# Kernel optimization log

Measured on AMD Instinct MI355X. Metric: run time of the kernel, lower is better.

The kernel has to match this reference:

```python
import jax, jax.numpy as jnp
import numpy as np

D_MODEL = 1024
NUM_HEADS = 16
HEAD_DIM = D_MODEL // NUM_HEADS
B, S = 2, 2048


def setup_inputs() -> dict:
    key = jax.random.key(0)
    ks = jax.random.split(key, 7)
    scale = 1.0 / np.sqrt(D_MODEL)
    return {
        "query": jax.random.normal(ks[0], (B, S, D_MODEL), jnp.float32),
        "key": jax.random.normal(ks[1], (B, S, D_MODEL), jnp.float32),
        "value": jax.random.normal(ks[2], (B, S, D_MODEL), jnp.float32),
        "Wq": jax.random.normal(ks[3], (D_MODEL, D_MODEL), jnp.float32) * scale,
        "Wk": jax.random.normal(ks[4], (D_MODEL, D_MODEL), jnp.float32) * scale,
        "Wv": jax.random.normal(ks[5], (D_MODEL, D_MODEL), jnp.float32) * scale,
        "Wo": jax.random.normal(ks[6], (D_MODEL, D_MODEL), jnp.float32) * scale,
    }


def reference(query, key, value, Wq, Wk, Wv, Wo):
    b, tl, _ = query.shape
    sl = key.shape[1]
    # Linear (no bias): x @ W.T, then split heads -> (B, H, L, Dh)
    def split_heads(x, L):
        return x.reshape(b, L, NUM_HEADS, HEAD_DIM).transpose(0, 2, 1, 3)
    Q = split_heads(query @ Wq.T, tl)
    K = split_heads(key @ Wk.T, sl)
    V = split_heads(value @ Wv.T, sl)
    scores = jnp.einsum("bhqd,bhkd->bhqk", Q, K) / jnp.sqrt(jnp.float32(HEAD_DIM))
    attn_weights = jax.nn.softmax(scores, axis=-1)
    # dropout is identity in eval mode
    context = jnp.einsum("bhqk,bhkd->bhqd", attn_weights, V)
    context = context.transpose(0, 2, 1, 3).reshape(b, tl, D_MODEL)
    output = context @ Wo.T
    return (output, attn_weights)
```

## Files before the change

kernel.cpp:

```cpp
#include <hip/hip_runtime.h>
#include <stdint.h>
#include <stddef.h>

#define D_MODEL 1024
#define NHEADS  16
#define HDIM    64
#define BB      2
#define SSEQ    2048

using bf16x8 = __attribute__((ext_vector_type(8))) short;
using f32x4  = __attribute__((ext_vector_type(4))) float;
using s16x4  = __attribute__((ext_vector_type(4))) short;

static __device__ __forceinline__ float b2f(short s) {
  union { float f; unsigned u; } v;
  v.u = ((unsigned)(unsigned short)s) << 16;
  return v.f;
}
static __device__ __forceinline__ short f2b(float f) {
  union { float f; unsigned u; } v;
  v.f = f;
  unsigned r = v.u + 0x7fffu + ((v.u >> 16) & 1u);
  return (short)(r >> 16);
}

static __device__ __forceinline__ void gload16(const void* g, void* l) {
  __builtin_amdgcn_global_load_lds(
      (const __attribute__((address_space(1))) unsigned int*)g,
      (__attribute__((address_space(3))) unsigned int*)l, 16, 0, 0);
}

__global__ __launch_bounds__(256) void k_cvt(const float* __restrict__ src,
                                             short* __restrict__ dst, int n4) {
  int i = blockIdx.x * blockDim.x + threadIdx.x;
  const int stride = gridDim.x * blockDim.x;
  for (; i < n4; i += stride) {
    const float4 v = ((const float4*)src)[i];
    s16x4 o;
    o[0] = f2b(v.x); o[1] = f2b(v.y); o[2] = f2b(v.z); o[3] = f2b(v.w);
    ((s16x4*)dst)[i] = o;
  }
}

template <bool F32OUT>
static __device__ __forceinline__ void gemm_bt_dev(
    const short* __restrict__ A, const short* __restrict__ W, void* __restrict__ Cv,
    int N, int K) {
  __shared__ short sA[128 * 32];
  __shared__ short sB[128 * 32];

  const int t  = threadIdx.x;
  const int l  = t & 63;
  const int w  = t >> 6;
  const int wm = w >> 1, wn = w & 1;
  const int g  = l >> 4, lr = l & 15;
  const int m0 = blockIdx.y * 128;
  const int n0 = blockIdx.x * 128;

  f32x4 acc[4][4];
#pragma unroll
  for (int i = 0; i < 4; ++i)
#pragma unroll
    for (int j = 0; j < 4; ++j) {
      acc[i][j][0] = 0.f; acc[i][j][1] = 0.f;
      acc[i][j][2] = 0.f; acc[i][j][3] = 0.f;
    }

  const int r0 = t >> 2;
  const int c0 = (t & 3) * 8;
  const short* ga0 = A + (size_t)(m0 + r0) * K + c0;
  const short* ga1 = A + (size_t)(m0 + 64 + r0) * K + c0;
  const short* gb0 = W + (size_t)(n0 + r0) * K + c0;
  const short* gb1 = W + (size_t)(n0 + 64 + r0) * K + c0;
  short* la0 = &sA[(t & ~63) * 8];
  short* la1 = la0 + 256 * 8;
  short* lb0 = &sB[(t & ~63) * 8];
  short* lb1 = lb0 + 256 * 8;

  for (int k0 = 0; k0 < K; k0 += 32) {
    __syncthreads();
    gload16(ga0 + k0, la0);
    gload16(ga1 + k0, la1);
    gload16(gb0 + k0, lb0);
    gload16(gb1 + k0, lb1);
    __syncthreads();

    bf16x8 af[4], bfr[4];
#pragma unroll
    for (int i = 0; i < 4; ++i)
      af[i] = *(const bf16x8*)&sA[(wm * 64 + i * 16 + lr) * 32 + g * 8];
#pragma unroll
    for (int i = 0; i < 4; ++i)
      bfr[i] = *(const bf16x8*)&sB[(wn * 64 + i * 16 + lr) * 32 + g * 8];
#pragma unroll
    for (int i = 0; i < 4; ++i)
#pragma unroll
      for (int j = 0; j < 4; ++j)
        acc[i][j] = __builtin_amdgcn_mfma_f32_16x16x32_bf16(af[i], bfr[j],
                                                            acc[i][j], 0, 0, 0);
  }

#pragma unroll
  for (int i = 0; i < 4; ++i)
#pragma unroll
    for (int j = 0; j < 4; ++j)
#pragma unroll
      for (int rr = 0; rr < 4; ++rr) {
        const int row = m0 + wm * 64 + i * 16 + g * 4 + rr;
        const int col = n0 + wn * 64 + j * 16 + lr;
        if (F32OUT)
          ((float*)Cv)[(size_t)row * N + col] = acc[i][j][rr];
        else
          ((short*)Cv)[(size_t)row * N + col] = f2b(acc[i][j][rr]);
      }
}

__global__ __launch_bounds__(256) void k_gemm_f32out(
    const short* __restrict__ A, const short* __restrict__ W,
    float* __restrict__ C, int N, int K) {
  gemm_bt_dev<true>(A, W, C, N, K);
}

__global__ __launch_bounds__(256) void k_gemm_qkv(
    const short* __restrict__ q, const short* __restrict__ k,
    const short* __restrict__ v, const short* __restrict__ wq,
    const short* __restrict__ wk, const short* __restrict__ wv,
    short* __restrict__ Qb, short* __restrict__ Kb, short* __restrict__ Vb) {
  const short *A, *W;
  short* C;
  if (blockIdx.z == 0)      { A = q; W = wq; C = Qb; }
  else if (blockIdx.z == 1) { A = k; W = wk; C = Kb; }
  else                      { A = v; W = wv; C = Vb; }
  gemm_bt_dev<false>(A, W, C, D_MODEL, D_MODEL);
}

__global__ __launch_bounds__(256) void k_transpose_v(
    const short* __restrict__ Vb, short* __restrict__ Vt) {
  __shared__ short tile[64][66];
  const int bh = blockIdx.x;
  const int b = bh >> 4, h = bh & 15;
  const int s0 = blockIdx.y * 64;
  const int t = threadIdx.x;
#pragma unroll
  for (int i = 0; i < 16; ++i) {
    int e = t + i * 256;
    int si = e >> 6, dj = e & 63;
    tile[si][dj] = Vb[((size_t)b * SSEQ + s0 + si) * D_MODEL + h * HDIM + dj];
  }
  __syncthreads();
#pragma unroll
  for (int i = 0; i < 16; ++i) {
    int e = t + i * 256;
    int dj = e >> 6, si = e & 63;
    Vt[((size_t)bh * HDIM + dj) * SSEQ + s0 + si] = tile[si][dj];
  }
}

__global__ __launch_bounds__(512) void k_attn(
    const short* __restrict__ Qb, const short* __restrict__ Kb,
    const short* __restrict__ Vt, float* __restrict__ attnO,
    short* __restrict__ ctx) {
  __shared__ short S[16 * SSEQ];
  __shared__ f32x4 red[4 * 64];
  const int t = threadIdx.x;
  const int l = t & 63, w = t >> 6;
  const int g = l >> 4, lr = l & 15;
  const int bh = blockIdx.y;
  const int b = bh >> 4, h = bh & 15;
  const int q0 = blockIdx.x * 16;

  const size_t qoff = ((size_t)b * SSEQ + q0 + lr) * D_MODEL + h * HDIM;
  const bf16x8 aq0 = *(const bf16x8*)&Qb[qoff + g * 8];
  const bf16x8 aq1 = *(const bf16x8*)&Qb[qoff + 32 + g * 8];

  const short* Kh = Kb + (size_t)b * SSEQ * D_MODEL + h * HDIM;

  for (int nt = 0; nt < 16; ++nt) {
    const int n0 = (w * 16 + nt) * 16;
    const short* krow = Kh + (size_t)(n0 + lr) * D_MODEL;
    const bf16x8 bk0 = *(const bf16x8*)&krow[g * 8];
    const bf16x8 bk1 = *(const bf16x8*)&krow[32 + g * 8];
    f32x4 acc;
    acc[0] = 0.f; acc[1] = 0.f; acc[2] = 0.f; acc[3] = 0.f;
    acc = __builtin_amdgcn_mfma_f32_16x16x32_bf16(aq0, bk0, acc, 0, 0, 0);
    acc = __builtin_amdgcn_mfma_f32_16x16x32_bf16(aq1, bk1, acc, 0, 0, 0);
#pragma unroll
    for (int rr = 0; rr < 4; ++rr) {
      const int row = g * 4 + rr;
      const int col = n0 + lr;
      const int pc = (col >> 3) ^ (row & 7);
      S[row * SSEQ + pc * 8 + (col & 7)] = f2b(acc[rr] * 0.125f);
    }
  }
  __syncthreads();

  const int r = t >> 5, j = t & 31;
  float mx = -1e30f;
  for (int i = 0; i < 8; ++i) {
    const int c = j + (i << 5);
    const int pc = c ^ (r & 7);
    const bf16x8 v = *(const bf16x8*)&S[r * SSEQ + pc * 8];
#pragma unroll
    for (int e = 0; e < 8; ++e) mx = fmaxf(mx, b2f(v[e]));
  }
#pragma unroll
  for (int mask = 1; mask < 32; mask <<= 1)
    mx = fmaxf(mx, __shfl_xor(mx, mask, 64));

  float sum = 0.f;
  for (int i = 0; i < 8; ++i) {
    const int c = j + (i << 5);
    const int pc = c ^ (r & 7);
    const bf16x8 v = *(const bf16x8*)&S[r * SSEQ + pc * 8];
#pragma unroll
    for (int e = 0; e < 8; ++e) sum += __expf(b2f(v[e]) - mx);
  }
#pragma unroll
  for (int mask = 1; mask < 32; mask <<= 1) sum += __shfl_xor(sum, mask, 64);
  const float inv = 1.f / sum;

  float* arow = attnO + ((size_t)bh * SSEQ + q0 + r) * SSEQ;
  for (int i = 0; i < 8; ++i) {
    const int c = j + (i << 5);
    const int pc = c ^ (r & 7);
    const bf16x8 v = *(const bf16x8*)&S[r * SSEQ + pc * 8];
    bf16x8 p;
#pragma unroll
    for (int e = 0; e < 8; ++e) {
      const float pe = __expf(b2f(v[e]) - mx) * inv;
      p[e] = f2b(pe);
      arow[(size_t)c * 8 + e] = pe;
    }
    *(bf16x8*)&S[r * SSEQ + pc * 8] = p;
  }
  __syncthreads();

  const short* Vh = Vt + (size_t)bh * HDIM * SSEQ;
  const int d0 = (w & 3) * 16;
  const int kh = w >> 2;
  f32x4 acc;
  acc[0] = 0.f; acc[1] = 0.f; acc[2] = 0.f; acc[3] = 0.f;
  const int sbeg = kh * (SSEQ / 2);
  for (int s0 = sbeg; s0 < sbeg + SSEQ / 2; s0 += 32) {
    const int pc = ((s0 >> 3) + g) ^ (lr & 7);
    const bf16x8 ap = *(const bf16x8*)&S[lr * SSEQ + pc * 8];
    const bf16x8 bv =
        *(const bf16x8*)&Vh[(size_t)(d0 + lr) * SSEQ + s0 + g * 8];
    acc = __builtin_amdgcn_mfma_f32_16x16x32_bf16(ap, bv, acc, 0, 0, 0);
  }
  if (kh == 1) red[(w & 3) * 64 + l] = acc;
  __syncthreads();
  if (kh == 0) {
    const f32x4 o = red[(w & 3) * 64 + l];
    acc[0] += o[0]; acc[1] += o[1]; acc[2] += o[2]; acc[3] += o[3];
#pragma unroll
    for (int rr = 0; rr < 4; ++rr) {
      const int qr = q0 + g * 4 + rr;
      ctx[((size_t)b * SSEQ + qr) * D_MODEL + h * HDIM + d0 + lr] =
          f2b(acc[rr]);
    }
  }
}

extern "C" void kernel_launch(void* const* d_in, const int* in_sizes, int n_in,
                              void* d_out, int out_size, void* d_ws,
                              size_t ws_size, hipStream_t stream) {
  const float* qf  = (const float*)d_in[0];
  const float* kf  = (const float*)d_in[1];
  const float* vf  = (const float*)d_in[2];
  const float* wqf = (const float*)d_in[3];
  const float* wkf = (const float*)d_in[4];
  const float* wvf = (const float*)d_in[5];
  const float* wof = (const float*)d_in[6];

  float* out  = (float*)d_out;
  float* attn = out + (size_t)BB * SSEQ * D_MODEL;

  const size_t NTOK = (size_t)BB * SSEQ;
  const size_t XN = NTOK * D_MODEL;
  const size_t WN = (size_t)D_MODEL * D_MODEL;

  short* qb  = (short*)d_ws;
  short* kb  = qb + XN;
  short* vb  = kb + XN;
  short* wqb = vb + XN;
  short* wkb = wqb + WN;
  short* wvb = wkb + WN;
  short* wob = wvb + WN;
  short* Qb  = wob + WN;
  short* Kb  = Qb + XN;
  short* Vb  = Kb + XN;
  short* Vt  = Vb + XN;
  short* ctx = Vt + XN;

  k_cvt<<<512, 256, 0, stream>>>(qf, qb, (int)(XN / 4));
  k_cvt<<<512, 256, 0, stream>>>(kf, kb, (int)(XN / 4));
  k_cvt<<<512, 256, 0, stream>>>(vf, vb, (int)(XN / 4));
  k_cvt<<<256, 256, 0, stream>>>(wqf, wqb, (int)(WN / 4));
  k_cvt<<<256, 256, 0, stream>>>(wkf, wkb, (int)(WN / 4));
  k_cvt<<<256, 256, 0, stream>>>(wvf, wvb, (int)(WN / 4));
  k_cvt<<<256, 256, 0, stream>>>(wof, wob, (int)(WN / 4));

  k_gemm_qkv<<<dim3(D_MODEL / 128, NTOK / 128, 3), 256, 0, stream>>>(
      qb, kb, vb, wqb, wkb, wvb, Qb, Kb, Vb);
  k_transpose_v<<<dim3(BB * NHEADS, SSEQ / 64), 256, 0, stream>>>(Vb, Vt);
  k_attn<<<dim3(SSEQ / 16, BB * NHEADS), 512, 0, stream>>>(Qb, Kb, Vt, attn,
                                                           ctx);
  k_gemm_f32out<<<dim3(D_MODEL / 128, NTOK / 128), 256, 0, stream>>>(
      ctx, wob, out, D_MODEL, D_MODEL);
}
```

Measured before the change: 898.4 us.

## Remap attention blocks for XCD locality, fuse row max, vectorize stores, unroll PV

```diff
diff --git a/kernel.cpp b/kernel.cpp
--- a/kernel.cpp
+++ b/kernel.cpp
@@ -162,12 +162,15 @@
     short* __restrict__ ctx) {
   __shared__ short S[16 * SSEQ];
   __shared__ f32x4 red[4 * 64];
+  __shared__ float rowmax[16][8];
   const int t = threadIdx.x;
   const int l = t & 63, w = t >> 6;
   const int g = l >> 4, lr = l & 15;
-  const int bh = blockIdx.y;
+  const int orig = blockIdx.x;
+  const int id = (orig & 7) * 512 + (orig >> 3);
+  const int q0 = (id & 127) * 16;
+  const int bh = id >> 7;
   const int b = bh >> 4, h = bh & 15;
-  const int q0 = blockIdx.x * 16;
 
   const size_t qoff = ((size_t)b * SSEQ + q0 + lr) * D_MODEL + h * HDIM;
   const bf16x8 aq0 = *(const bf16x8*)&Qb[qoff + g * 8];
@@ -175,37 +178,49 @@
 
   const short* Kh = Kb + (size_t)b * SSEQ * D_MODEL + h * HDIM;
 
-  for (int nt = 0; nt < 16; ++nt) {
-    const int n0 = (w * 16 + nt) * 16;
-    const short* krow = Kh + (size_t)(n0 + lr) * D_MODEL;
-    const bf16x8 bk0 = *(const bf16x8*)&krow[g * 8];
-    const bf16x8 bk1 = *(const bf16x8*)&krow[32 + g * 8];
-    f32x4 acc;
-    acc[0] = 0.f; acc[1] = 0.f; acc[2] = 0.f; acc[3] = 0.f;
-    acc = __builtin_amdgcn_mfma_f32_16x16x32_bf16(aq0, bk0, acc, 0, 0, 0);
-    acc = __builtin_amdgcn_mfma_f32_16x16x32_bf16(aq1, bk1, acc, 0, 0, 0);
+  f32x4 pmax;
+  pmax[0] = -1e30f; pmax[1] = -1e30f; pmax[2] = -1e30f; pmax[3] = -1e30f;
+  for (int nt = 0; nt < 16; nt += 2) {
+    const int n0a = (w * 16 + nt) * 16;
+    const int n0b = n0a + 16;
+    const short* kra = Kh + (size_t)(n0a + lr) * D_MODEL;
+    const short* krb = Kh + (size_t)(n0b + lr) * D_MODEL;
+    const bf16x8 ka0 = *(const bf16x8*)&kra[g * 8];
+    const bf16x8 ka1 = *(const bf16x8*)&kra[32 + g * 8];
+    const bf16x8 kb0 = *(const bf16x8*)&krb[g * 8];
+    const bf16x8 kb1 = *(const bf16x8*)&krb[32 + g * 8];
+    f32x4 acca, accb;
+    acca[0] = 0.f; acca[1] = 0.f; acca[2] = 0.f; acca[3] = 0.f;
+    accb[0] = 0.f; accb[1] = 0.f; accb[2] = 0.f; accb[3] = 0.f;
+    acca = __builtin_amdgcn_mfma_f32_16x16x32_bf16(aq0, ka0, acca, 0, 0, 0);
+    acca = __builtin_amdgcn_mfma_f32_16x16x32_bf16(aq1, ka1, acca, 0, 0, 0);
+    accb = __builtin_amdgcn_mfma_f32_16x16x32_bf16(aq0, kb0, accb, 0, 0, 0);
+    accb = __builtin_amdgcn_mfma_f32_16x16x32_bf16(aq1, kb1, accb, 0, 0, 0);
 #pragma unroll
     for (int rr = 0; rr < 4; ++rr) {
       const int row = g * 4 + rr;
-      const int col = n0 + lr;
-      const int pc = (col >> 3) ^ (row & 7);
-      S[row * SSEQ + pc * 8 + (col & 7)] = f2b(acc[rr] * 0.125f);
-    }
-  }
+      const float sa = acca[rr] * 0.125f;
+      const float sb = accb[rr] * 0.125f;
+      pmax[rr] = fmaxf(pmax[rr], fmaxf(sa, sb));
+      const int ca = n0a + lr, cb = n0b + lr;
+      S[row * SSEQ + (((ca >> 3) ^ (row & 7)) << 3) + (ca & 7)] = f2b(sa);
+      S[row * SSEQ + (((cb >> 3) ^ (row & 7)) << 3) + (cb & 7)] = f2b(sb);
+    }
+  }
+#pragma unroll
+  for (int mask = 1; mask < 16; mask <<= 1)
+#pragma unroll
+    for (int rr = 0; rr < 4; ++rr)
+      pmax[rr] = fmaxf(pmax[rr], __shfl_xor(pmax[rr], mask, 64));
+  if (lr == 0)
+#pragma unroll
+    for (int rr = 0; rr < 4; ++rr) rowmax[g * 4 + rr][w] = pmax[rr];
   __syncthreads();
 
   const int r = t >> 5, j = t & 31;
-  float mx = -1e30f;
-  for (int i = 0; i < 8; ++i) {
-    const int c = j + (i << 5);
-    const int pc = c ^ (r & 7);
-    const bf16x8 v = *(const bf16x8*)&S[r * SSEQ + pc * 8];
-#pragma unroll
-    for (int e = 0; e < 8; ++e) mx = fmaxf(mx, b2f(v[e]));
-  }
-#pragma unroll
-  for (int mask = 1; mask < 32; mask <<= 1)
-    mx = fmaxf(mx, __shfl_xor(mx, mask, 64));
+  float mx = rowmax[r][0];
+#pragma unroll
+  for (int ww = 1; ww < 8; ++ww) mx = fmaxf(mx, rowmax[r][ww]);
 
   float sum = 0.f;
   for (int i = 0; i < 8; ++i) {
@@ -225,12 +240,23 @@
     const int pc = c ^ (r & 7);
     const bf16x8 v = *(const bf16x8*)&S[r * SSEQ + pc * 8];
     bf16x8 p;
-#pragma unroll
-    for (int e = 0; e < 8; ++e) {
-      const float pe = __expf(b2f(v[e]) - mx) * inv;
-      p[e] = f2b(pe);
-      arow[(size_t)c * 8 + e] = pe;
-    }
+    float4 w0, w1;
+    {
+      const float p0 = __expf(b2f(v[0]) - mx) * inv;
+      const float p1 = __expf(b2f(v[1]) - mx) * inv;
+      const float p2 = __expf(b2f(v[2]) - mx) * inv;
+      const float p3 = __expf(b2f(v[3]) - mx) * inv;
+      w0.x = p0; w0.y = p1; w0.z = p2; w0.w = p3;
+      p[0] = f2b(p0); p[1] = f2b(p1); p[2] = f2b(p2); p[3] = f2b(p3);
+      const float p4 = __expf(b2f(v[4]) - mx) * inv;
+      const float p5 = __expf(b2f(v[5]) - mx) * inv;
+      const float p6 = __expf(b2f(v[6]) - mx) * inv;
+      const float p7 = __expf(b2f(v[7]) - mx) * inv;
+      w1.x = p4; w1.y = p5; w1.z = p6; w1.w = p7;
+      p[4] = f2b(p4); p[5] = f2b(p5); p[6] = f2b(p6); p[7] = f2b(p7);
+    }
+    *(float4*)(arow + (size_t)c * 8) = w0;
+    *(float4*)(arow + (size_t)c * 8 + 4) = w1;
     *(bf16x8*)&S[r * SSEQ + pc * 8] = p;
   }
   __syncthreads();
@@ -241,12 +267,18 @@
   f32x4 acc;
   acc[0] = 0.f; acc[1] = 0.f; acc[2] = 0.f; acc[3] = 0.f;
   const int sbeg = kh * (SSEQ / 2);
-  for (int s0 = sbeg; s0 < sbeg + SSEQ / 2; s0 += 32) {
-    const int pc = ((s0 >> 3) + g) ^ (lr & 7);
-    const bf16x8 ap = *(const bf16x8*)&S[lr * SSEQ + pc * 8];
-    const bf16x8 bv =
-        *(const bf16x8*)&Vh[(size_t)(d0 + lr) * SSEQ + s0 + g * 8];
-    acc = __builtin_amdgcn_mfma_f32_16x16x32_bf16(ap, bv, acc, 0, 0, 0);
+  for (int s0 = sbeg; s0 < sbeg + SSEQ / 2; s0 += 128) {
+    bf16x8 ap[4], bv[4];
+#pragma unroll
+    for (int u = 0; u < 4; ++u) {
+      const int ss = s0 + u * 32;
+      const int pc = ((ss >> 3) + g) ^ (lr & 7);
+      ap[u] = *(const bf16x8*)&S[lr * SSEQ + pc * 8];
+      bv[u] = *(const bf16x8*)&Vh[(size_t)(d0 + lr) * SSEQ + ss + g * 8];
+    }
+#pragma unroll
+    for (int u = 0; u < 4; ++u)
+      acc = __builtin_amdgcn_mfma_f32_16x16x32_bf16(ap[u], bv[u], acc, 0, 0, 0);
   }
   if (kh == 1) red[(w & 3) * 64 + l] = acc;
   __syncthreads();
@@ -304,8 +336,7 @@
   k_gemm_qkv<<<dim3(D_MODEL / 128, NTOK / 128, 3), 256, 0, stream>>>(
       qb, kb, vb, wqb, wkb, wvb, Qb, Kb, Vb);
   k_transpose_v<<<dim3(BB * NHEADS, SSEQ / 64), 256, 0, stream>>>(Vb, Vt);
-  k_attn<<<dim3(SSEQ / 16, BB * NHEADS), 512, 0, stream>>>(Qb, Kb, Vt, attn,
-                                                           ctx);
+  k_attn<<<4096, 512, 0, stream>>>(Qb, Kb, Vt, attn, ctx);
   k_gemm_f32out<<<dim3(D_MODEL / 128, NTOK / 128), 256, 0, stream>>>(
       ctx, wob, out, D_MODEL, D_MODEL);
 }
```

After: 885.7 us. No clear change (-1.4%).
